# Optimization experiments

Measured on AMD Instinct MI355X. Metric: run time of the kernel, lower is better.

Reference implementation:

```python
import jax, jax.numpy as jnp
import numpy as np

EMB_DIM = 768
NUM_HEADS = 12
HEAD_DIM = EMB_DIM // NUM_HEADS
B, S = 8, 1024


def setup_inputs() -> dict:
    key = jax.random.key(0)
    ks = jax.random.split(key, 8)
    q = jax.random.normal(ks[0], (B, S, EMB_DIM), dtype=jnp.float32)
    k = jax.random.normal(ks[1], (B, S, EMB_DIM), dtype=jnp.float32)
    v = jax.random.normal(ks[2], (B, S, EMB_DIM), dtype=jnp.float32)
    # Per-head projection weights, torch nn.Linear layout [out_dim, in_dim]
    xav = float(np.sqrt(6.0 / (HEAD_DIM + HEAD_DIM)))
    Wq = jax.random.uniform(ks[3], (NUM_HEADS, HEAD_DIM, HEAD_DIM), jnp.float32, -xav, xav)
    Wk = jax.random.uniform(ks[4], (NUM_HEADS, HEAD_DIM, HEAD_DIM), jnp.float32, -xav, xav)
    Wv = jax.random.uniform(ks[5], (NUM_HEADS, HEAD_DIM, HEAD_DIM), jnp.float32, -xav, xav)
    # Output projection (torch Linear default init scale not critical for correctness baseline)
    bound = float(1.0 / np.sqrt(EMB_DIM))
    Wo = jax.random.uniform(ks[6], (EMB_DIM, EMB_DIM), jnp.float32, -bound, bound)
    bo = jax.random.uniform(ks[7], (EMB_DIM,), jnp.float32, -bound, bound)
    return {"q": q, "k": k, "v": v, "Wq": Wq, "Wk": Wk, "Wv": Wv, "Wo": Wo, "bo": bo}


def reference(q, k, v, Wq, Wk, Wv, Wo, bo):
    b, s, _ = q.shape
    # split heads: [B, S, E] -> [B, H, S, d]
    def split(x):
        return x.reshape(b, s, NUM_HEADS, HEAD_DIM).transpose(0, 2, 1, 3)
    qh, kh, vh = split(q), split(k), split(v)
    # per-head linear (torch: y = x @ W^T), vectorized over heads
    Q = jnp.einsum('bhsd,hod->bhso', qh, Wq)
    K = jnp.einsum('bhsd,hod->bhso', kh, Wk)
    V = jnp.einsum('bhsd,hod->bhso', vh, Wv)
    scale = 1.0 / jnp.sqrt(jnp.float32(HEAD_DIM))
    scores = jnp.einsum('bhqd,bhkd->bhqk', Q, K) * scale  # [B,H,S,S]
    weights = jax.nn.softmax(scores, axis=-1)
    attn = jnp.einsum('bhqk,bhkd->bhqd', weights, V)
    # merge heads: [B,H,S,d] -> [B,S,E]
    attn = attn.transpose(0, 2, 1, 3).reshape(b, s, EMB_DIM)
    return attn @ Wo.T + bo
```

## Files before the change

kernel.cpp:

```cpp
#include <hip/hip_runtime.h>
#include <hip/hip_bf16.h>

#define BB 8
#define SS 1024
#define EE 768
#define HH 12
#define DD 64
#define NT (BB*SS)

typedef __attribute__((ext_vector_type(8))) short bf16x8;
typedef __attribute__((ext_vector_type(4))) float f32x4;

__device__ __forceinline__ ushort f2bf(float f) {
  union { float f; unsigned u; } x; x.f = f;
  unsigned r = x.u + 0x7fffu + ((x.u >> 16) & 1u);
  return (ushort)(r >> 16);
}

__device__ __forceinline__ unsigned cvtpk(float a, float b) {
  unsigned r;
  asm("v_cvt_pk_bf16_f32 %0, %1, %2" : "=v"(r) : "v"(a), "v"(b));
  return r;
}

__device__ __forceinline__ void gl2lds(const void* g, void* l) {
  __builtin_amdgcn_global_load_lds(
      (const __attribute__((address_space(1))) unsigned int*)g,
      (__attribute__((address_space(3))) unsigned int*)l, 16, 0, 0);
}

__global__ void cvt_weights(const float* __restrict__ Wq, const float* __restrict__ Wk,
                            const float* __restrict__ Wv, const float* __restrict__ Wo,
                            ushort* __restrict__ Wqb, ushort* __restrict__ Wkb,
                            ushort* __restrict__ Wvb, ushort* __restrict__ Wob) {
  int i = blockIdx.x * blockDim.x + threadIdx.x;
  const int NW = HH*DD*DD;
  if (i < NW) { Wqb[i] = f2bf(Wq[i]); Wkb[i] = f2bf(Wk[i]); Wvb[i] = f2bf(Wv[i]); }
  if (i < EE*EE) Wob[i] = f2bf(Wo[i]);
}

__global__ __launch_bounds__(256) void proj_qkv(
    const float* __restrict__ q, const float* __restrict__ k, const float* __restrict__ v,
    const ushort* __restrict__ Wqb, const ushort* __restrict__ Wkb, const ushort* __restrict__ Wvb,
    ushort* __restrict__ Qb, ushort* __restrict__ Kb, ushort* __restrict__ Vt) {
  int bid = blockIdx.x;
  int m  = bid / (BB*HH*(SS/64));
  int r  = bid % (BB*HH*(SS/64));
  int bh = r / (SS/64);
  int st = r % (SS/64);

  const float*  x = (m==0 ? q : (m==1 ? k : v)) + ((size_t)((bh/HH)*SS + st*64))*EE + (bh%HH)*DD;
  const ushort* W = (m==0 ? Wqb : (m==1 ? Wkb : Wvb)) + (bh%HH)*DD*DD;

  int tid = threadIdx.x;
  int w = tid >> 6, l = tid & 63;
  int lr = l & 15, lg = l >> 4;

  bf16x8 a[2];
  const float* xr = x + (size_t)(w*16 + lr)*EE;
#pragma unroll
  for (int ks = 0; ks < 2; ++ks) {
    f32x4 t0 = *(const f32x4*)(xr + ks*32 + lg*8);
    f32x4 t1 = *(const f32x4*)(xr + ks*32 + lg*8 + 4);
    bf16x8 av;
#pragma unroll
    for (int j = 0; j < 4; ++j) { av[j] = (short)f2bf(t0[j]); av[4+j] = (short)f2bf(t1[j]); }
    a[ks] = av;
  }

  f32x4 acc[4] = {};
  if (m == 2) {
#pragma unroll
    for (int f = 0; f < 4; ++f) {
      bf16x8 b0 = *(const bf16x8*)(W + (f*16 + lr)*DD + lg*8);
      bf16x8 b1 = *(const bf16x8*)(W + (f*16 + lr)*DD + 32 + lg*8);
      acc[f] = __builtin_amdgcn_mfma_f32_16x16x32_bf16(a[0], b0, acc[f], 0, 0, 0);
      acc[f] = __builtin_amdgcn_mfma_f32_16x16x32_bf16(a[1], b1, acc[f], 0, 0, 0);
    }
    int posb = st*64 + 32*(w>>1) + 8*lg + 4*(w&1);
#pragma unroll
    for (int f = 0; f < 4; ++f) {
      ushort2 p0, p1;
      *(unsigned*)&p0 = cvtpk(acc[f][0], acc[f][1]);
      *(unsigned*)&p1 = cvtpk(acc[f][2], acc[f][3]);
      ushort4 pk; pk.x = p0.x; pk.y = p0.y; pk.z = p1.x; pk.w = p1.y;
      *(ushort4*)(Vt + ((size_t)bh*DD + f*16 + lr)*SS + posb) = pk;
    }
  } else {
#pragma unroll
    for (int f = 0; f < 4; ++f) {
      bf16x8 b0 = *(const bf16x8*)(W + (f*16 + lr)*DD + lg*8);
      bf16x8 b1 = *(const bf16x8*)(W + (f*16 + lr)*DD + 32 + lg*8);
      acc[f] = __builtin_amdgcn_mfma_f32_16x16x32_bf16(b0, a[0], acc[f], 0, 0, 0);
      acc[f] = __builtin_amdgcn_mfma_f32_16x16x32_bf16(b1, a[1], acc[f], 0, 0, 0);
    }
    float qscale = (m == 0) ? 0.18033688011112042f : 1.0f;
    ushort* dst = (m == 0 ? Qb : Kb) + ((size_t)bh*SS + st*64 + w*16 + lr)*DD;
#pragma unroll
    for (int f = 0; f < 4; ++f) {
      ushort2 p0, p1;
      *(unsigned*)&p0 = cvtpk(acc[f][0]*qscale, acc[f][1]*qscale);
      *(unsigned*)&p1 = cvtpk(acc[f][2]*qscale, acc[f][3]*qscale);
      ushort4 pk; pk.x = p0.x; pk.y = p0.y; pk.z = p1.x; pk.w = p1.y;
      *(ushort4*)(dst + f*16 + lg*4) = pk;
    }
  }
}

__global__ __launch_bounds__(256) void attn_fwd(
    const ushort* __restrict__ Qb, const ushort* __restrict__ Kb,
    const ushort* __restrict__ Vt, ushort* __restrict__ attn) {
  __shared__ uint4 ldsq[2048];
  char* ldsb = (char*)ldsq;

  int bid = blockIdx.x;
  int bh = bid % (BB*HH);
  int qt = bid / (BB*HH);
  int b = bh / HH, h = bh % HH;
  int tid = threadIdx.x, w = tid >> 6, l = tid & 63;
  int lr = l & 15, lg = l >> 4;

  const ushort* Qp0 = Qb + ((size_t)bh*SS + qt*128 + w*32 + lr)*DD;
  bf16x8 bq[2][2];
  bq[0][0] = *(const bf16x8*)(Qp0 + lg*8);
  bq[0][1] = *(const bf16x8*)(Qp0 + 32 + lg*8);
  bq[1][0] = *(const bf16x8*)(Qp0 + 16*DD + lg*8);
  bq[1][1] = *(const bf16x8*)(Qp0 + 16*DD + 32 + lg*8);

  const ushort* Kbh = Kb + (size_t)bh*SS*DD;
  const ushort* Vbh = Vt + (size_t)bh*DD*SS;

  float l_run[2] = {0.f, 0.f};
  f32x4 o[2][4] = {};

#define STAGE(bufidx, kt) do {                                                   \
    char* LK_ = ldsb + (bufidx)*16384;                                           \
    const ushort* ksrc = Kbh + ((size_t)((kt)*64 + w*16 + lr))*DD + lg*8;        \
    const ushort* vsrc = Vbh + ((size_t)(w*16 + lr))*SS + (kt)*64 + lg*8;        \
    gl2lds(ksrc,      LK_ + tid*16);                                             \
    gl2lds(ksrc + 32, LK_ + 4096 + tid*16);                                      \
    gl2lds(vsrc,      LK_ + 8192 + tid*16);                                      \
    gl2lds(vsrc + 32, LK_ + 12288 + tid*16);                                     \
  } while (0)

  STAGE(0, 0);
  for (int kt = 0; kt < 16; ++kt) {
    const int cur = kt & 1;
    const char* LK_ = ldsb + cur*16384;
    const char* LV_ = LK_ + 8192;

    asm volatile("s_waitcnt vmcnt(0)" ::: "memory");
    __builtin_amdgcn_s_barrier();
    __builtin_amdgcn_sched_barrier(0);

    if (kt < 15) STAGE(cur ^ 1, kt + 1);

    f32x4 st0[4] = {}, st1[4] = {};
    __builtin_amdgcn_s_setprio(1);
#pragma unroll
    for (int f = 0; f < 4; ++f) {
      bf16x8 k0 = *(const bf16x8*)(LK_ + f*1024 + l*16);
      bf16x8 k1 = *(const bf16x8*)(LK_ + 4096 + f*1024 + l*16);
      st0[f] = __builtin_amdgcn_mfma_f32_16x16x32_bf16(k0, bq[0][0], st0[f], 0, 0, 0);
      st0[f] = __builtin_amdgcn_mfma_f32_16x16x32_bf16(k1, bq[0][1], st0[f], 0, 0, 0);
      st1[f] = __builtin_amdgcn_mfma_f32_16x16x32_bf16(k0, bq[1][0], st1[f], 0, 0, 0);
      st1[f] = __builtin_amdgcn_mfma_f32_16x16x32_bf16(k1, bq[1][1], st1[f], 0, 0, 0);
    }
    __builtin_amdgcn_s_setprio(0);

    union { bf16x8 v; unsigned u[4]; } pba[2], pbb[2];
#pragma unroll
    for (int s = 0; s < 2; ++s) {
      f32x4* st = (s == 0) ? st0 : st1;
      float rs = 0.f;
#pragma unroll
      for (int f = 0; f < 4; ++f) {
#pragma unroll
        for (int j = 0; j < 4; ++j) {
          float pv = __builtin_amdgcn_exp2f(st[f][j]);
          st[f][j] = pv; rs += pv;
        }
      }
      l_run[s] += rs;
      pba[s].u[0] = cvtpk(st[0][0], st[0][1]); pba[s].u[1] = cvtpk(st[0][2], st[0][3]);
      pba[s].u[2] = cvtpk(st[1][0], st[1][1]); pba[s].u[3] = cvtpk(st[1][2], st[1][3]);
      pbb[s].u[0] = cvtpk(st[2][0], st[2][1]); pbb[s].u[1] = cvtpk(st[2][2], st[2][3]);
      pbb[s].u[2] = cvtpk(st[3][0], st[3][1]); pbb[s].u[3] = cvtpk(st[3][2], st[3][3]);
    }

    __builtin_amdgcn_s_setprio(1);
#pragma unroll
    for (int f = 0; f < 4; ++f) {
      bf16x8 va = *(const bf16x8*)(LV_ + f*1024 + l*16);
      bf16x8 vc = *(const bf16x8*)(LV_ + 4096 + f*1024 + l*16);
      o[0][f] = __builtin_amdgcn_mfma_f32_16x16x32_bf16(va, pba[0].v, o[0][f], 0, 0, 0);
      o[0][f] = __builtin_amdgcn_mfma_f32_16x16x32_bf16(vc, pbb[0].v, o[0][f], 0, 0, 0);
      o[1][f] = __builtin_amdgcn_mfma_f32_16x16x32_bf16(va, pba[1].v, o[1][f], 0, 0, 0);
      o[1][f] = __builtin_amdgcn_mfma_f32_16x16x32_bf16(vc, pbb[1].v, o[1][f], 0, 0, 0);
    }
    __builtin_amdgcn_s_setprio(0);
  }
#undef STAGE

#pragma unroll
  for (int s = 0; s < 2; ++s) {
    float rs = l_run[s];
    rs += __shfl_xor(rs, 16, 64);
    rs += __shfl_xor(rs, 32, 64);
    float inv = 1.0f / rs;
    ushort* orow = attn + ((size_t)(b*SS + qt*128 + w*32 + s*16 + lr))*EE + h*DD;
#pragma unroll
    for (int f = 0; f < 4; ++f) {
      ushort4 pkd;
      pkd.x = f2bf(o[s][f][0] * inv);
      pkd.y = f2bf(o[s][f][1] * inv);
      pkd.z = f2bf(o[s][f][2] * inv);
      pkd.w = f2bf(o[s][f][3] * inv);
      *(ushort4*)(orow + f*16 + lg*4) = pkd;
    }
  }
}

__global__ __launch_bounds__(256) void out_proj(
    const ushort* __restrict__ attn, const ushort* __restrict__ Wob,
    const float* __restrict__ bo, float* __restrict__ out) {
  __shared__ uint4 ldsq[3072];
  char* ldsb = (char*)ldsq;

  int bid = blockIdx.x;
  int mt = bid & 127;
  int nt = bid >> 7;
  int tid = threadIdx.x, w = tid >> 6, l = tid & 63;
  int lr = l & 15, lg = l >> 4;

  int rS = tid >> 3;
  int cSw = (((tid & 7) * 16) ^ ((rS & 7) << 4)) >> 1;

  const ushort* Abase = attn + ((size_t)mt*64)*EE;
  const ushort* Bbase = Wob + ((size_t)nt*128)*EE;

#define OSTAGE(bufidx, kt) do {                                                  \
    char* LA_ = ldsb + (bufidx)*24576;                                           \
    char* LB_ = LA_ + 8192;                                                      \
    const ushort* asrc = Abase + (kt)*64 + cSw;                                  \
    const ushort* bsrc = Bbase + (kt)*64 + cSw;                                  \
    gl2lds(asrc + (size_t)rS*EE,        LA_ + tid*16);                           \
    gl2lds(asrc + (size_t)(rS+32)*EE,   LA_ + 4096 + tid*16);                    \
    gl2lds(bsrc + (size_t)rS*EE,        LB_ + tid*16);                           \
    gl2lds(bsrc + (size_t)(rS+32)*EE,   LB_ + 4096 + tid*16);                    \
    gl2lds(bsrc + (size_t)(rS+64)*EE,   LB_ + 8192 + tid*16);                    \
    gl2lds(bsrc + (size_t)(rS+96)*EE,   LB_ + 12288 + tid*16);                   \
  } while (0)

  f32x4 acc[4][2] = {};

#define OCOMPUTE(bufidx) do {                                                    \
    const char* LA_ = ldsb + (bufidx)*24576;                                     \
    const char* LB_ = LA_ + 8192;                                                \
    bf16x8 af[4][2], bf[2][2];                                                   \
    _Pragma("unroll")                                                            \
    for (int f = 0; f < 4; ++f) {                                                \
      int row = f*16 + lr; int sw = (row & 7) << 4;                              \
      af[f][0] = *(const bf16x8*)(LA_ + row*128 + ((lg*16) ^ sw));               \
      af[f][1] = *(const bf16x8*)(LA_ + row*128 + ((64 + lg*16) ^ sw));          \
    }                                                                            \
    _Pragma("unroll")                                                            \
    for (int g = 0; g < 2; ++g) {                                                \
      int row = w*32 + g*16 + lr; int sw = (row & 7) << 4;                       \
      bf[g][0] = *(const bf16x8*)(LB_ + row*128 + ((lg*16) ^ sw));               \
      bf[g][1] = *(const bf16x8*)(LB_ + row*128 + ((64 + lg*16) ^ sw));          \
    }                                                                            \
    _Pragma("unroll")                                                            \
    for (int f = 0; f < 4; ++f) {                                                \
      _Pragma("unroll")                                                          \
      for (int g = 0; g < 2; ++g) {                                              \
        acc[f][g] = __builtin_amdgcn_mfma_f32_16x16x32_bf16(af[f][0], bf[g][0], acc[f][g], 0, 0, 0); \
        acc[f][g] = __builtin_amdgcn_mfma_f32_16x16x32_bf16(af[f][1], bf[g][1], acc[f][g], 0, 0, 0); \
      }                                                                          \
    }                                                                            \
  } while (0)

  OSTAGE(0, 0);
  __syncthreads();
  for (int kt = 0; kt < EE/64; ++kt) {
    if (kt < EE/64 - 1) OSTAGE((kt + 1) & 1, kt + 1);
    OCOMPUTE(kt & 1);
    __syncthreads();
  }
#undef OSTAGE
#undef OCOMPUTE

#pragma unroll
  for (int g = 0; g < 2; ++g) {
    int col = nt*128 + w*32 + g*16 + lr;
    float bias = bo[col];
#pragma unroll
    for (int f = 0; f < 4; ++f) {
#pragma unroll
      for (int j = 0; j < 4; ++j) {
        int row = mt*64 + f*16 + lg*4 + j;
        out[(size_t)row*EE + col] = acc[f][g][j] + bias;
      }
    }
  }
}

extern "C" void kernel_launch(void* const* d_in, const int* in_sizes, int n_in,
                              void* d_out, int out_size, void* d_ws, size_t ws_size,
                              hipStream_t stream) {
  (void)in_sizes; (void)n_in; (void)out_size; (void)ws_size;
  const float* q  = (const float*)d_in[0];
  const float* k  = (const float*)d_in[1];
  const float* v  = (const float*)d_in[2];
  const float* Wq = (const float*)d_in[3];
  const float* Wk = (const float*)d_in[4];
  const float* Wv = (const float*)d_in[5];
  const float* Wo = (const float*)d_in[6];
  const float* bo = (const float*)d_in[7];
  float* out = (float*)d_out;

  char* ws = (char*)d_ws;
  const size_t SZ = (size_t)BB*HH*SS*DD*2;
  ushort* Qb   = (ushort*)(ws);
  ushort* Kb   = (ushort*)(ws + SZ);
  ushort* Vt   = (ushort*)(ws + 2*SZ);
  ushort* attn = (ushort*)(ws + 3*SZ);
  ushort* Wqb  = (ushort*)(ws + 4*SZ);
  ushort* Wkb  = (ushort*)(ws + 4*SZ +   98304);
  ushort* Wvb  = (ushort*)(ws + 4*SZ + 2*98304);
  ushort* Wob  = (ushort*)(ws + 4*SZ + 3*98304);

  cvt_weights<<<(EE*EE + 255)/256, 256, 0, stream>>>(Wq, Wk, Wv, Wo, Wqb, Wkb, Wvb, Wob);
  proj_qkv<<<3*BB*HH*(SS/64), 256, 0, stream>>>(q, k, v, Wqb, Wkb, Wvb, Qb, Kb, Vt);
  attn_fwd<<<BB*HH*(SS/128), 256, 0, stream>>>(Qb, Kb, Vt, attn);
  out_proj<<<(NT/64)*(EE/128), 256, 0, stream>>>(attn, Wob, bo, out);
}
```

Baseline: 92.02 us.

## Triple-buffer K/V loads in attention and compute row sums via MFMA

Moves the attention K/V staging from double to triple buffering in LDS, prefetching two tiles ahead and waiting only on the older load group, so global-to-LDS latency overlaps more compute. Also replaces the scalar per-lane exp-sum accumulation and final cross-lane shuffles with extra MFMAs against a ones vector, which accumulate the softmax denominator in bf16-rounded probabilities. This raises LDS use per block, which may lower occupancy, and adds four MFMAs per tile.

```diff
diff --git a/kernel.cpp b/kernel.cpp
--- a/kernel.cpp
+++ b/kernel.cpp
@@ -110,7 +110,7 @@
 __global__ __launch_bounds__(256) void attn_fwd(
     const ushort* __restrict__ Qb, const ushort* __restrict__ Kb,
     const ushort* __restrict__ Vt, ushort* __restrict__ attn) {
-  __shared__ uint4 ldsq[2048];
+  __shared__ uint4 ldsq[3072];
   char* ldsb = (char*)ldsq;
 
   int bid = blockIdx.x;
@@ -130,7 +130,10 @@
   const ushort* Kbh = Kb + (size_t)bh*SS*DD;
   const ushort* Vbh = Vt + (size_t)bh*DD*SS;
 
-  float l_run[2] = {0.f, 0.f};
+  const short ONE = (short)0x3F80;
+  bf16x8 ones = {ONE, ONE, ONE, ONE, ONE, ONE, ONE, ONE};
+
+  f32x4 lsum[2] = {};
   f32x4 o[2][4] = {};
 
 #define STAGE(bufidx, kt) do {                                                   \
@@ -144,16 +147,19 @@
   } while (0)
 
   STAGE(0, 0);
+  STAGE(1, 1);
+  int bi = 0;
   for (int kt = 0; kt < 16; ++kt) {
-    const int cur = kt & 1;
-    const char* LK_ = ldsb + cur*16384;
+    const char* LK_ = ldsb + bi*16384;
     const char* LV_ = LK_ + 8192;
 
-    asm volatile("s_waitcnt vmcnt(0)" ::: "memory");
+    if (kt < 15) { asm volatile("s_waitcnt vmcnt(4)" ::: "memory"); }
+    else         { asm volatile("s_waitcnt vmcnt(0)" ::: "memory"); }
     __builtin_amdgcn_s_barrier();
     __builtin_amdgcn_sched_barrier(0);
 
-    if (kt < 15) STAGE(cur ^ 1, kt + 1);
+    int pi = bi + 2; if (pi >= 3) pi -= 3;
+    if (kt < 14) STAGE(pi, kt + 2);
 
     f32x4 st0[4] = {}, st1[4] = {};
     __builtin_amdgcn_s_setprio(1);
@@ -172,16 +178,11 @@
 #pragma unroll
     for (int s = 0; s < 2; ++s) {
       f32x4* st = (s == 0) ? st0 : st1;
-      float rs = 0.f;
 #pragma unroll
       for (int f = 0; f < 4; ++f) {
 #pragma unroll
-        for (int j = 0; j < 4; ++j) {
-          float pv = __builtin_amdgcn_exp2f(st[f][j]);
-          st[f][j] = pv; rs += pv;
-        }
+        for (int j = 0; j < 4; ++j) st[f][j] = __builtin_amdgcn_exp2f(st[f][j]);
       }
-      l_run[s] += rs;
       pba[s].u[0] = cvtpk(st[0][0], st[0][1]); pba[s].u[1] = cvtpk(st[0][2], st[0][3]);
       pba[s].u[2] = cvtpk(st[1][0], st[1][1]); pba[s].u[3] = cvtpk(st[1][2], st[1][3]);
       pbb[s].u[0] = cvtpk(st[2][0], st[2][1]); pbb[s].u[1] = cvtpk(st[2][2], st[2][3]);
@@ -198,16 +199,19 @@
       o[1][f] = __builtin_amdgcn_mfma_f32_16x16x32_bf16(va, pba[1].v, o[1][f], 0, 0, 0);
       o[1][f] = __builtin_amdgcn_mfma_f32_16x16x32_bf16(vc, pbb[1].v, o[1][f], 0, 0, 0);
     }
+    lsum[0] = __builtin_amdgcn_mfma_f32_16x16x32_bf16(ones, pba[0].v, lsum[0], 0, 0, 0);
+    lsum[0] = __builtin_amdgcn_mfma_f32_16x16x32_bf16(ones, pbb[0].v, lsum[0], 0, 0, 0);
+    lsum[1] = __builtin_amdgcn_mfma_f32_16x16x32_bf16(ones, pba[1].v, lsum[1], 0, 0, 0);
+    lsum[1] = __builtin_amdgcn_mfma_f32_16x16x32_bf16(ones, pbb[1].v, lsum[1], 0, 0, 0);
     __builtin_amdgcn_s_setprio(0);
+
+    bi = (bi == 2) ? 0 : bi + 1;
   }
 #undef STAGE
 
 #pragma unroll
   for (int s = 0; s < 2; ++s) {
-    float rs = l_run[s];
-    rs += __shfl_xor(rs, 16, 64);
-    rs += __shfl_xor(rs, 32, 64);
-    float inv = 1.0f / rs;
+    float inv = 1.0f / lsum[s][0];
     ushort* orow = attn + ((size_t)(b*SS + qt*128 + w*32 + s*16 + lr))*EE + h*DD;
 #pragma unroll
     for (int f = 0; f < 4; ++f) {
```

Result: faster. 90.21 us (-2.0%).
